# Performance work log

Hardware: AMD Instinct MI355X
Metric: run time of the kernel (lower is better)

The kernel has to match this reference:

```python
import jax, jax.numpy as jnp
import numpy as np

HID = 1024
DEPTH = 2

def _rhn_layer(x, Win, bin_, Wh, bh, Wt, bt):
    # x: [B, T, in]; returns outputs [B, T, H]
    B = x.shape[0]
    h0 = jnp.zeros((B, HID), dtype=x.dtype)
    xt = jnp.swapaxes(x, 0, 1)  # [T, B, in]

    def step(h_prev, x_t):
        h = x_t @ Win + bin_
        for i in range(DEPTH):
            t_gate = jax.nn.sigmoid(h @ Wt[i] + bt[i])
            h_layer = jnp.tanh(h @ Wh[i] + bh[i])
            h = t_gate * h_layer + (1.0 - t_gate) * h
        h_new = h + h_prev
        return h_new, h_new

    _, outs = jax.lax.scan(step, h0, xt)  # [T, B, H]
    return jnp.swapaxes(outs, 0, 1)


def setup_inputs() -> dict:
    key = jax.random.key(0)
    ks = jax.random.split(key, 16)
    B, T, IN, H, OUT = 64, 256, 128, HID, 128
    s = lambda fan_in: 1.0 / np.sqrt(fan_in)
    d = {}
    d["x"] = jax.random.normal(ks[0], (B, T, IN), dtype=jnp.float32)
    # layer 0 (input_size=IN)
    d["l0_Win"] = jax.random.uniform(ks[1], (IN, H), minval=-s(IN), maxval=s(IN))
    d["l0_bin"] = jax.random.uniform(ks[2], (H,), minval=-s(IN), maxval=s(IN))
    d["l0_Wh"] = jax.random.uniform(ks[3], (DEPTH, H, H), minval=-s(H), maxval=s(H))
    d["l0_bh"] = jax.random.uniform(ks[4], (DEPTH, H), minval=-s(H), maxval=s(H))
    d["l0_Wt"] = jax.random.uniform(ks[5], (DEPTH, H, H), minval=-s(H), maxval=s(H))
    d["l0_bt"] = jax.random.uniform(ks[6], (DEPTH, H), minval=-s(H), maxval=s(H))
    # layer 1 (input_size=H)
    d["l1_Win"] = jax.random.uniform(ks[7], (H, H), minval=-s(H), maxval=s(H))
    d["l1_bin"] = jax.random.uniform(ks[8], (H,), minval=-s(H), maxval=s(H))
    d["l1_Wh"] = jax.random.uniform(ks[9], (DEPTH, H, H), minval=-s(H), maxval=s(H))
    d["l1_bh"] = jax.random.uniform(ks[10], (DEPTH, H), minval=-s(H), maxval=s(H))
    d["l1_Wt"] = jax.random.uniform(ks[11], (DEPTH, H, H), minval=-s(H), maxval=s(H))
    d["l1_bt"] = jax.random.uniform(ks[12], (DEPTH, H), minval=-s(H), maxval=s(H))
    # final fc
    d["fc_W"] = jax.random.uniform(ks[13], (H, OUT), minval=-s(H), maxval=s(H))
    d["fc_b"] = jax.random.uniform(ks[14], (OUT,), minval=-s(H), maxval=s(H))
    return d


def reference(x, l0_Win, l0_bin, l0_Wh, l0_bh, l0_Wt, l0_bt,
              l1_Win, l1_bin, l1_Wh, l1_bh, l1_Wt, l1_bt, fc_W, fc_b):
    out = _rhn_layer(x, l0_Win, l0_bin, l0_Wh, l0_bh, l0_Wt, l0_bt)
    out = _rhn_layer(out, l1_Win, l1_bin, l1_Wh, l1_bh, l1_Wt, l1_bt)
    # forecast_horizon = 1 -> last time step only
    out = out[:, -1:, :] @ fc_W + fc_b  # [B, 1, OUT]
    return out
```

## Files before the change

kernel.cpp:

```cpp
#include <hip/hip_runtime.h>

typedef unsigned short u16;
typedef unsigned int u32;
typedef __bf16 bf16x8 __attribute__((ext_vector_type(8)));
typedef float floatx4 __attribute__((ext_vector_type(4)));

#define HID 1024
#define BATCH 64
#define SEQ 256
#define INDIM 128
#define OUTDIM 128
#define MROWS (BATCH*SEQ)
#define CUMP 140

__device__ __forceinline__ float b2f(u16 u) {
    union { u32 u; float f; } v; v.u = ((u32)u) << 16; return v.f;
}
__device__ __forceinline__ u16 f2b(float f) {
    union { float f; u32 u; } v; v.f = f;
    u32 x = v.u;
    x += 0x7fffu + ((x >> 16) & 1u);
    return (u16)(x >> 16);
}
__device__ __forceinline__ float sigm(float x) { return 1.f / (1.f + __expf(-x)); }
__device__ __forceinline__ float tanh_f(float x) { return 2.f / (1.f + __expf(-2.f * x)) - 1.f; }

__device__ __forceinline__ void gld16(const u16* g, u16* l) {
    __builtin_amdgcn_global_load_lds(
        (const __attribute__((address_space(1))) void*)g,
        (__attribute__((address_space(3))) void*)l, 16, 0, 0);
}

__device__ __forceinline__ void bar_sync() {
    asm volatile("" ::: "memory");
    __builtin_amdgcn_s_barrier();
    asm volatile("" ::: "memory");
}
template <int N>
__device__ __forceinline__ void vm_bar() {
    asm volatile("s_waitcnt vmcnt(%0)" :: "n"(N) : "memory");
    __builtin_amdgcn_s_barrier();
    asm volatile("" ::: "memory");
}

__device__ __forceinline__ int is_fp32(const u16* probe, int tid) {
    const int lane = tid & 63;
    const int e = (probe[lane * 7] >> 7) & 0xff;
    return __ballot(e >= 127) != 0ULL;
}

struct PrepList {
    const void* ts[10]; u16* td[10]; int tR[10]; int tC[10]; long toff[10];
    const void* cs[8];  u16* cd[8];  int cn[8];
};

__global__ void prep18(PrepList P, const u16* __restrict__ probe) {
    const int tid  = threadIdx.x;
    const int fp32 = is_fp32(probe, tid);
    const int z = blockIdx.z;
    if (z < 10) {
        const int tx = tid & 31, ty = tid >> 5;
        const void* src = P.ts[z];
        u16*        dst = P.td[z];
        const int R  = P.tR[z];
        const int Cc = P.tC[z];
        const long zo = P.toff[z];
        const int tr = blockIdx.y * 32, tc = blockIdx.x * 32;
        if (tr >= R || tc >= Cc) return;
        __align__(16) __shared__ u16 t[32][33];
#pragma unroll
        for (int i = 0; i < 4; ++i) {
            const int r = ty + i * 8;
            const long e = zo + (long)(tr + r) * Cc + tc + tx;
            u16 v;
            if (fp32) v = f2b(((const float*)src)[e]);
            else      v = ((const u16*)src)[e];
            t[r][tx] = v;
        }
        __syncthreads();
#pragma unroll
        for (int i = 0; i < 4; ++i) {
            const int r = ty + i * 8;
            dst[(size_t)(tc + r) * R + tr + tx] = t[tx][r];
        }
    } else {
        const int c = z - 10;
        const int n = P.cn[c];
        const int lin = blockIdx.y * gridDim.x + blockIdx.x;
        const int stride = gridDim.x * gridDim.y * 256;
        for (int i = lin * 256 + tid; i < n; i += stride) {
            u16 o;
            if (fp32) o = f2b(((const float*)P.cs[c])[i]);
            else      o = ((const u16*)P.cs[c])[i];
            P.cd[c][i] = o;
        }
    }
}

__device__ __forceinline__ void tile_swizzle(int& m0, int& n0) {
    const int lin = blockIdx.y * gridDim.x + blockIdx.x;
    const int xcd = lin & 7;
    const int loc = lin >> 3;
    m0 = (xcd * 16 + (loc & 15)) * 128;
    n0 = (loc >> 4) * 128;
}

__device__ __forceinline__ void tile_swizzle8(int& m0, int& n0) {
    const int lin = blockIdx.x;
    const int xcd = lin & 7;
    const int loc = lin >> 3;
    m0 = (xcd * 8 + (loc & 7)) * 256;
    n0 = (loc >> 3) * 128;
}

__global__ __launch_bounds__(256, 2) void gemm128(
    const u16* __restrict__ A, const u16* __restrict__ BT,
    const u16* __restrict__ bias, u16* __restrict__ C,
    int M, int N, int K)
{
    __align__(16) __shared__ u16 As[128 * 64];
    __align__(16) __shared__ u16 Bs[128 * 64];

    const int tid  = threadIdx.x;
    const int lane = tid & 63;
    const int wid  = tid >> 6;
    const int wr   = wid >> 1;
    const int wc   = wid & 1;

    int m0, n0;
    tile_swizzle(m0, n0);

    floatx4 acc[4][4] = {};

    const int srow = lane >> 3;
    const int scol = 8 * ((lane & 7) ^ (lane >> 3));
    const int cb   = wid * 4;
    const u16* Ag[4]; const u16* Bg[4];
    u16 *Al[4], *Bl[4];
#pragma unroll
    for (int j = 0; j < 4; ++j) {
        const int c = cb + j;
        const int r = c * 8 + srow;
        Ag[j] = A  + (size_t)(m0 + r) * K + scol;
        Bg[j] = BT + (size_t)(n0 + r) * K + scol;
        Al[j] = As + c * 512;
        Bl[j] = Bs + c * 512;
    }

    const int quad = lane >> 4;
    const int l16  = lane & 15;
    const int swz  = l16 & 7;

    const int nk = K >> 6;
    for (int kt = 0; kt < nk; ++kt) {
        __syncthreads();
#pragma unroll
        for (int j = 0; j < 4; ++j) {
            gld16(Ag[j], Al[j]);  gld16(Bg[j], Bl[j]);
            Ag[j] += 64; Bg[j] += 64;
        }
        __syncthreads();

#pragma unroll
        for (int kk = 0; kk < 2; ++kk) {
            const int slot = ((kk * 4 + quad) ^ swz) * 8;
            bf16x8 af[4], bfr[4];
#pragma unroll
            for (int i = 0; i < 4; ++i) {
                af[i]  = *(const bf16x8*)(As + (wr * 64 + i * 16 + l16) * 64 + slot);
                bfr[i] = *(const bf16x8*)(Bs + (wc * 64 + i * 16 + l16) * 64 + slot);
            }
#pragma unroll
            for (int i = 0; i < 4; ++i)
#pragma unroll
                for (int j = 0; j < 4; ++j)
                    acc[i][j] = __builtin_amdgcn_mfma_f32_16x16x32_bf16(af[i], bfr[j], acc[i][j], 0, 0, 0);
        }
    }

#pragma unroll
    for (int i = 0; i < 4; ++i) {
        const int rowb = m0 + wr * 64 + i * 16 + quad * 4;
#pragma unroll
        for (int j = 0; j < 4; ++j) {
            const int col = n0 + wc * 64 + j * 16 + l16;
            const float bv = b2f(bias[col]);
#pragma unroll
            for (int r = 0; r < 4; ++r)
                C[(size_t)(rowb + r) * N + col] = f2b(acc[i][j][r] + bv);
        }
    }
}

__global__ __launch_bounds__(256, 2) void gemm_wp_bias(
    const u16* __restrict__ At, const u16* __restrict__ Ah,
    const u16* __restrict__ BT,
    const u16* __restrict__ binv, const u16* __restrict__ bt0, const u16* __restrict__ bh0,
    u16* __restrict__ Ct, u16* __restrict__ Ch,
    u16* __restrict__ obt, u16* __restrict__ obh)
{
    const int tid = threadIdx.x;
    if (blockIdx.z == 1) {
        __shared__ float part[256];
        const u16* tW = blockIdx.y ? Ah : At;
        const u16* bo = blockIdx.y ? bh0 : bt0;
        u16*       ob = blockIdx.y ? obh : obt;
        const int j  = blockIdx.x * 128 + (tid & 127);
        const int kh = tid >> 7;
        const u16* row = tW + (size_t)j * HID + kh * 512;
        float acc = 0.f;
        for (int k = 0; k < 512; k += 8) {
            uint4 wv = *(const uint4*)(row + k);
            uint4 bv = *(const uint4*)(binv + kh * 512 + k);
            const u16* w = (const u16*)&wv;
            const u16* b = (const u16*)&bv;
#pragma unroll
            for (int e = 0; e < 8; ++e) acc += b2f(b[e]) * b2f(w[e]);
        }
        part[tid] = acc;
        __syncthreads();
        if (tid < 128)
            ob[j] = f2b(part[tid] + part[tid + 128] + b2f(bo[j]));
        return;
    }

    const u16* A = blockIdx.y ? Ah : At;
    u16*       C = blockIdx.y ? Ch : Ct;
    const int m0 = blockIdx.x * 128;
    const int K = HID, N = 128;

    __align__(16) __shared__ u16 As[128 * 64];
    __align__(16) __shared__ u16 Bs[128 * 64];

    const int lane = tid & 63;
    const int wid  = tid >> 6;
    const int wr   = wid >> 1;
    const int wc   = wid & 1;

    floatx4 acc[4][4] = {};

    const int srow = lane >> 3;
    const int scol = 8 * ((lane & 7) ^ (lane >> 3));
    const int cb   = wid * 4;
    const u16* Ag[4]; const u16* Bg[4];
    u16 *Al[4], *Bl[4];
#pragma unroll
    for (int j = 0; j < 4; ++j) {
        const int c = cb + j;
        const int r = c * 8 + srow;
        Ag[j] = A  + (size_t)(m0 + r) * K + scol;
        Bg[j] = BT + (size_t)r * K + scol;
        Al[j] = As + c * 512;
        Bl[j] = Bs + c * 512;
    }

    const int quad = lane >> 4;
    const int l16  = lane & 15;
    const int swz  = l16 & 7;

    for (int kt = 0; kt < (K >> 6); ++kt) {
        __syncthreads();
#pragma unroll
        for (int j = 0; j < 4; ++j) {
            gld16(Ag[j], Al[j]);  gld16(Bg[j], Bl[j]);
            Ag[j] += 64; Bg[j] += 64;
        }
        __syncthreads();

#pragma unroll
        for (int kk = 0; kk < 2; ++kk) {
            const int slot = ((kk * 4 + quad) ^ swz) * 8;
            bf16x8 af[4], bfr[4];
#pragma unroll
            for (int i = 0; i < 4; ++i) {
                af[i]  = *(const bf16x8*)(As + (wr * 64 + i * 16 + l16) * 64 + slot);
                bfr[i] = *(const bf16x8*)(Bs + (wc * 64 + i * 16 + l16) * 64 + slot);
            }
#pragma unroll
            for (int i = 0; i < 4; ++i)
#pragma unroll
                for (int j = 0; j < 4; ++j)
                    acc[i][j] = __builtin_amdgcn_mfma_f32_16x16x32_bf16(af[i], bfr[j], acc[i][j], 0, 0, 0);
        }
    }

#pragma unroll
    for (int i = 0; i < 4; ++i) {
        const int rowb = m0 + wr * 64 + i * 16 + quad * 4;
#pragma unroll
        for (int j = 0; j < 4; ++j) {
            const int col = wc * 64 + j * 16 + l16;
#pragma unroll
            for (int r = 0; r < 4; ++r)
                C[(size_t)(rowb + r) * N + col] = f2b(acc[i][j][r]);
        }
    }
}

__global__ __launch_bounds__(512, 2) void gemm_hw3(
    const u16* __restrict__ A,
    const u16* __restrict__ WtP,
    const u16* __restrict__ WhP,
    const u16* __restrict__ WiT,
    const u16* __restrict__ bpt, const u16* __restrict__ bph,
    const u16* __restrict__ bin,
    u16* __restrict__ Hout,
    int M, int N, int K)
{
    __align__(16) __shared__ u16 As [128 * 64];
    __align__(16) __shared__ u16 Bts[128 * 64];
    __align__(16) __shared__ u16 Bhs[128 * 64];
    __align__(16) __shared__ u16 Bis[128 * 64];

    const int tid  = threadIdx.x;
    const int lane = tid & 63;
    const int wid  = tid >> 6;
    const int wm   = wid >> 2;
    const int wn   = wid & 3;

    int m0, n0;
    tile_swizzle(m0, n0);

    floatx4 acct[4][2] = {};
    floatx4 acch[4][2] = {};
    floatx4 acci[4][2] = {};

    const int srow = lane >> 3;
    const int scol = 8 * ((lane & 7) ^ srow);
    const u16* Ag[2]; const u16* Tg[2]; const u16* Hg[2]; const u16* Ig[2];
    u16 *Al[2], *Tl[2], *Hl[2], *Il[2];
#pragma unroll
    for (int j = 0; j < 2; ++j) {
        const int c = wid * 2 + j;
        const int r = c * 8 + srow;
        Ag[j] = A   + (size_t)(m0 + r) * K + scol;
        Tg[j] = WtP + (size_t)(n0 + r) * K + scol;
        Hg[j] = WhP + (size_t)(n0 + r) * K + scol;
        Ig[j] = WiT + (size_t)(n0 + r) * K + scol;
        Al[j] = As  + c * 512;
        Tl[j] = Bts + c * 512;
        Hl[j] = Bhs + c * 512;
        Il[j] = Bis + c * 512;
    }

    const int quad = lane >> 4;
    const int l16  = lane & 15;
    const int swz  = l16 & 7;

    const int nk = K >> 6;
    for (int kt = 0; kt < nk; ++kt) {
        __syncthreads();
#pragma unroll
        for (int j = 0; j < 2; ++j) {
            gld16(Ag[j], Al[j]);  gld16(Tg[j], Tl[j]);
            gld16(Hg[j], Hl[j]);  gld16(Ig[j], Il[j]);
            Ag[j] += 64; Tg[j] += 64; Hg[j] += 64; Ig[j] += 64;
        }
        __syncthreads();

#pragma unroll
        for (int kk = 0; kk < 2; ++kk) {
            const int slot = ((kk * 4 + quad) ^ swz) * 8;
            bf16x8 af[4], btf[2], bhf[2], bif[2];
#pragma unroll
            for (int i = 0; i < 4; ++i)
                af[i] = *(const bf16x8*)(As + (wm * 64 + i * 16 + l16) * 64 + slot);
#pragma unroll
            for (int j = 0; j < 2; ++j) {
                btf[j] = *(const bf16x8*)(Bts + (wn * 32 + j * 16 + l16) * 64 + slot);
                bhf[j] = *(const bf16x8*)(Bhs + (wn * 32 + j * 16 + l16) * 64 + slot);
                bif[j] = *(const bf16x8*)(Bis + (wn * 32 + j * 16 + l16) * 64 + slot);
            }
#pragma unroll
            for (int i = 0; i < 4; ++i)
#pragma unroll
                for (int j = 0; j < 2; ++j) {
                    acct[i][j] = __builtin_amdgcn_mfma_f32_16x16x32_bf16(af[i], btf[j], acct[i][j], 0, 0, 0);
                    acch[i][j] = __builtin_amdgcn_mfma_f32_16x16x32_bf16(af[i], bhf[j], acch[i][j], 0, 0, 0);
                    acci[i][j] = __builtin_amdgcn_mfma_f32_16x16x32_bf16(af[i], bif[j], acci[i][j], 0, 0, 0);
                }
        }
    }

#pragma unroll
    for (int i = 0; i < 4; ++i) {
        const int rowb = m0 + wm * 64 + i * 16 + quad * 4;
#pragma unroll
        for (int j = 0; j < 2; ++j) {
            const int col = n0 + wn * 32 + j * 16 + l16;
            const float biv = b2f(bin[col]);
            const float btv = b2f(bpt[col]);
            const float bhv = b2f(bph[col]);
#pragma unroll
            for (int r = 0; r < 4; ++r) {
                const float h  = acci[i][j][r] + biv;
                const float tg = sigm(acct[i][j][r] + btv);
                const float hl = tanh_f(acch[i][j][r] + bhv);
                Hout[(size_t)(rowb + r) * N + col] = f2b(h + tg * (hl - h));
            }
        }
    }
}

__global__ __launch_bounds__(256, 2) void gemm_hw(
    const u16* __restrict__ A,
    const u16* __restrict__ WtT,
    const u16* __restrict__ WhT,
    const u16* __restrict__ bt, const u16* __restrict__ bh,
    u16* __restrict__ Hout,
    int M, int N, int K)
{
    __align__(16) __shared__ u16 As [128 * 64];
    __align__(16) __shared__ u16 Bts[128 * 64];
    __align__(16) __shared__ u16 Bhs[128 * 64];

    const int tid  = threadIdx.x;
    const int lane = tid & 63;
    const int wid  = tid >> 6;
    const int wr   = wid >> 1;
    const int wc   = wid & 1;

    int m0, n0;
    tile_swizzle(m0, n0);

    floatx4 acct[4][4] = {};
    floatx4 acch[4][4] = {};

    const int srow = lane >> 3;
    const int scol = 8 * ((lane & 7) ^ (lane >> 3));
    const int cb   = wid * 4;
    const u16* Ag[4]; const u16* Tg[4]; const u16* Hg[4];
    u16 *Al[4], *Tl[4], *Hl[4];
#pragma unroll
    for (int j = 0; j < 4; ++j) {
        const int c = cb + j;
        const int r = c * 8 + srow;
        Ag[j] = A   + (size_t)(m0 + r) * K + scol;
        Tg[j] = WtT + (size_t)(n0 + r) * K + scol;
        Hg[j] = WhT + (size_t)(n0 + r) * K + scol;
        Al[j] = As  + c * 512;
        Tl[j] = Bts + c * 512;
        Hl[j] = Bhs + c * 512;
    }

    const int quad = lane >> 4;
    const int l16  = lane & 15;
    const int swz  = l16 & 7;

    const int nk = K >> 6;
    for (int kt = 0; kt < nk; ++kt) {
        __syncthreads();
#pragma unroll
        for (int j = 0; j < 4; ++j) {
            gld16(Ag[j], Al[j]);  gld16(Tg[j], Tl[j]);  gld16(Hg[j], Hl[j]);
            Ag[j] += 64; Tg[j] += 64; Hg[j] += 64;
        }
        __syncthreads();

#pragma unroll
        for (int kk = 0; kk < 2; ++kk) {
            const int slot = ((kk * 4 + quad) ^ swz) * 8;
            bf16x8 af[4], btf[4], bhf[4];
#pragma unroll
            for (int i = 0; i < 4; ++i) {
                af[i]  = *(const bf16x8*)(As  + (wr * 64 + i * 16 + l16) * 64 + slot);
                btf[i] = *(const bf16x8*)(Bts + (wc * 64 + i * 16 + l16) * 64 + slot);
                bhf[i] = *(const bf16x8*)(Bhs + (wc * 64 + i * 16 + l16) * 64 + slot);
            }
#pragma unroll
            for (int i = 0; i < 4; ++i)
#pragma unroll
                for (int j = 0; j < 4; ++j) {
                    acct[i][j] = __builtin_amdgcn_mfma_f32_16x16x32_bf16(af[i], btf[j], acct[i][j], 0, 0, 0);
                    acch[i][j] = __builtin_amdgcn_mfma_f32_16x16x32_bf16(af[i], bhf[j], acch[i][j], 0, 0, 0);
                }
        }
    }

#pragma unroll
    for (int i = 0; i < 4; ++i) {
        const int rowb = m0 + wr * 64 + i * 16 + quad * 4;
#pragma unroll
        for (int j = 0; j < 4; ++j) {
            const int col = n0 + wc * 64 + j * 16 + l16;
            const float btv = b2f(bt[col]);
            const float bhv = b2f(bh[col]);
#pragma unroll
            for (int r = 0; r < 4; ++r) {
                const size_t idx = (size_t)(rowb + r) * N + col;
                const float hold = b2f(A[idx]);
                const float tg = sigm(acct[i][j][r] + btv);
                const float hl = tanh_f(acch[i][j][r] + bhv);
                Hout[idx] = f2b(hold + tg * (hl - hold));
            }
        }
    }
}

__global__ __launch_bounds__(256, 2) void gemm_hw_sum(
    const u16* __restrict__ A,
    const u16* __restrict__ WtT,
    const u16* __restrict__ WhT,
    const u16* __restrict__ bt, const u16* __restrict__ bh,
    float* __restrict__ hpart,
    int M, int N, int K)
{
    __align__(16) __shared__ u16 As [128 * 64];
    __align__(16) __shared__ u16 Bts[128 * 64];
    __align__(16) __shared__ u16 Bhs[128 * 64];

    const int tid  = threadIdx.x;
    const int lane = tid & 63;
    const int wid  = tid >> 6;
    const int wr   = wid >> 1;
    const int wc   = wid & 1;

    int m0, n0;
    tile_swizzle(m0, n0);

    floatx4 acct[4][4] = {};
    floatx4 acch[4][4] = {};

    const int srow = lane >> 3;
    const int scol = 8 * ((lane & 7) ^ (lane >> 3));
    const int cb   = wid * 4;
    const u16* Ag[4]; const u16* Tg[4]; const u16* Hg[4];
    u16 *Al[4], *Tl[4], *Hl[4];
#pragma unroll
    for (int j = 0; j < 4; ++j) {
        const int c = cb + j;
        const int r = c * 8 + srow;
        Ag[j] = A   + (size_t)(m0 + r) * K + scol;
        Tg[j] = WtT + (size_t)(n0 + r) * K + scol;
        Hg[j] = WhT + (size_t)(n0 + r) * K + scol;
        Al[j] = As  + c * 512;
        Tl[j] = Bts + c * 512;
        Hl[j] = Bhs + c * 512;
    }

    const int quad = lane >> 4;
    const int l16  = lane & 15;
    const int swz  = l16 & 7;

    const int nk = K >> 6;
    for (int kt = 0; kt < nk; ++kt) {
        __syncthreads();
#pragma unroll
        for (int j = 0; j < 4; ++j) {
            gld16(Ag[j], Al[j]);  gld16(Tg[j], Tl[j]);  gld16(Hg[j], Hl[j]);
            Ag[j] += 64; Tg[j] += 64; Hg[j] += 64;
        }
        __syncthreads();

#pragma unroll
        for (int kk = 0; kk < 2; ++kk) {
            const int slot = ((kk * 4 + quad) ^ swz) * 8;
            bf16x8 af[4], btf[4], bhf[4];
#pragma unroll
            for (int i = 0; i < 4; ++i) {
                af[i]  = *(const bf16x8*)(As  + (wr * 64 + i * 16 + l16) * 64 + slot);
                btf[i] = *(const bf16x8*)(Bts + (wc * 64 + i * 16 + l16) * 64 + slot);
                bhf[i] = *(const bf16x8*)(Bhs + (wc * 64 + i * 16 + l16) * 64 + slot);
            }
#pragma unroll
            for (int i = 0; i < 4; ++i)
#pragma unroll
                for (int j = 0; j < 4; ++j) {
                    acct[i][j] = __builtin_amdgcn_mfma_f32_16x16x32_bf16(af[i], btf[j], acct[i][j], 0, 0, 0);
                    acch[i][j] = __builtin_amdgcn_mfma_f32_16x16x32_bf16(af[i], bhf[j], acch[i][j], 0, 0, 0);
                }
        }
    }

    const int b    = m0 >> 8;
    const int slot = ((m0 >> 7) & 1) * 2 + wr;
#pragma unroll
    for (int j = 0; j < 4; ++j) {
        const int col = n0 + wc * 64 + j * 16 + l16;
        const float btv = b2f(bt[col]);
        const float bhv = b2f(bh[col]);
        float colsum = 0.f;
#pragma unroll
        for (int i = 0; i < 4; ++i) {
            const int rowb = m0 + wr * 64 + i * 16 + quad * 4;
#pragma unroll
            for (int r = 0; r < 4; ++r) {
                const size_t idx = (size_t)(rowb + r) * N + col;
                const float hold = b2f(A[idx]);
                const float tg = sigm(acct[i][j][r] + btv);
                const float hl = tanh_f(acch[i][j][r] + bhv);
                colsum += hold + tg * (hl - hold);
            }
        }
        colsum += __shfl_xor(colsum, 16, 64);
        colsum += __shfl_xor(colsum, 32, 64);
        if (quad == 0)
            hpart[((size_t)(slot * BATCH + b)) * HID + col] = colsum;
    }
}

__device__ __forceinline__ void hw8_mainloop(
    u16* lds,
    const u16* __restrict__ A, const u16* __restrict__ WtT, const u16* __restrict__ WhT,
    int m0, int n0, int K,
    floatx4 (&acct)[4][4], floatx4 (&acch)[4][4])
{
    const int tid  = threadIdx.x;
    const int lane = tid & 63;
    const int wid  = tid >> 6;
    const int wr   = wid >> 1;
    const int wc   = wid & 1;

    const int srow = lane >> 3;
    const int scol = 8 * ((lane & 7) ^ srow);

    const u16* Ag = A   + (size_t)(m0 + wid * 32 + srow) * K + scol;
    const u16* Tg = WtT + (size_t)(n0 + wid * 16 + srow) * K + scol;
    const u16* Hg = WhT + (size_t)(n0 + wid * 16 + srow) * K + scol;
    const size_t K8 = (size_t)K * 8;

    u16* dA = lds + wid * 2048;
    u16* dT = lds + 16384 + wid * 1024;
    u16* dH = lds + 24576 + wid * 1024;

    const int quad = lane >> 4;
    const int l16  = lane & 15;
    const int swz  = l16 & 7;
    const int s0 = (quad ^ swz) * 8;
    const int s1 = ((4 + quad) ^ swz) * 8;
    const int ra = wr * 64 + l16;
    const int rb = wc * 64 + l16;

    gld16(Tg,           dT);
    gld16(Tg +     K8,  dT + 512);
    gld16(Ag,           dA);
    gld16(Ag +     K8,  dA + 512);
    gld16(Ag + 2 * K8,  dA + 1024);
    gld16(Ag + 3 * K8,  dA + 1536);
    gld16(Hg,           dH);
    gld16(Hg +     K8,  dH + 512);
    Ag += 64; Tg += 64; Hg += 64;
    vm_bar<2>();

    const int nk = K >> 6;
    for (int kt = 0; kt < nk; ++kt) {
        const int  cur = kt & 1;
        const int  nb  = (cur ^ 1) * 32768;
        const bool pf  = (kt + 1 < nk);
        const u16* Sa = lds + cur * 32768;
        const u16* St = Sa + 16384;
        const u16* Sh = Sa + 24576;

        bf16x8 af0[4], af1[4], bq[4];

#pragma unroll
        for (int i = 0; i < 4; ++i) {
            af0[i] = *(const bf16x8*)(Sa + (ra + i * 16) * 64 + s0);
            bq[i]  = *(const bf16x8*)(St + (rb + i * 16) * 64 + s0);
        }
        if (pf) {
            gld16(Tg,      dT + nb);  gld16(Tg + K8, dT + nb + 512);
            gld16(Ag,      dA + nb);  gld16(Ag + K8, dA + nb + 512);
        }
        bar_sync();
        __builtin_amdgcn_s_setprio(1);
#pragma unroll
        for (int i = 0; i < 4; ++i)
#pragma unroll
            for (int j = 0; j < 4; ++j)
                acct[i][j] = __builtin_amdgcn_mfma_f32_16x16x32_bf16(af0[i], bq[j], acct[i][j], 0, 0, 0);
        __builtin_amdgcn_s_setprio(0);

#pragma unroll
        for (int i = 0; i < 4; ++i) {
            af1[i] = *(const bf16x8*)(Sa + (ra + i * 16) * 64 + s1);
            bq[i]  = *(const bf16x8*)(St + (rb + i * 16) * 64 + s1);
        }
        if (pf) {
            gld16(Ag + 2 * K8, dA + nb + 1024);
            gld16(Ag + 3 * K8, dA + nb + 1536);
            vm_bar<6>();
        } else {
            vm_bar<0>();
        }
        __builtin_amdgcn_s_setprio(1);
#pragma unroll
        for (int i = 0; i < 4; ++i)
#pragma unroll
            for (int j = 0; j < 4; ++j)
                acct[i][j] = __builtin_amdgcn_mfma_f32_16x16x32_bf16(af1[i], bq[j], acct[i][j], 0, 0, 0);
        __builtin_amdgcn_s_setprio(0);

#pragma unroll
        for (int i = 0; i < 4; ++i)
            bq[i] = *(const bf16x8*)(Sh + (rb + i * 16) * 64 + s0);
        bar_sync();
        __builtin_amdgcn_s_setprio(1);
#pragma unroll
        for (int i = 0; i < 4; ++i)
#pragma unroll
            for (int j = 0; j < 4; ++j)
                acch[i][j] = __builtin_amdgcn_mfma_f32_16x16x32_bf16(af0[i], bq[j], acch[i][j], 0, 0, 0);
        __builtin_amdgcn_s_setprio(0);

#pragma unroll
        for (int i = 0; i < 4; ++i)
            bq[i] = *(const bf16x8*)(Sh + (rb + i * 16) * 64 + s1);
        if (pf) {
            gld16(Hg,      dH + nb);
            gld16(Hg + K8, dH + nb + 512);
            vm_bar<2>();
        } else {
            bar_sync();
        }
        __builtin_amdgcn_s_setprio(1);
#pragma unroll
        for (int i = 0; i < 4; ++i)
#pragma unroll
            for (int j = 0; j < 4; ++j)
                acch[i][j] = __builtin_amdgcn_mfma_f32_16x16x32_bf16(af1[i], bq[j], acch[i][j], 0, 0, 0);
        __builtin_amdgcn_s_setprio(0);

        Ag += 64; Tg += 64; Hg += 64;
    }
}

__global__ __launch_bounds__(512, 2) void gemm_hw8_cum(
    const u16* __restrict__ A,
    const u16* __restrict__ WtT,
    const u16* __restrict__ WhT,
    const u16* __restrict__ bt, const u16* __restrict__ bh,
    u16* __restrict__ Y,
    int M, int N, int K)
{
    __align__(16) __shared__ u16 lds[65536];
    __shared__ float tot[512];

    int m0, n0;
    tile_swizzle8(m0, n0);

    floatx4 acct[4][4] = {};
    floatx4 acch[4][4] = {};
    hw8_mainloop(lds, A, WtT, WhT, m0, n0, K, acct, acch);

    const int tid  = threadIdx.x;
    const int lane = tid & 63;
    const int wid  = tid >> 6;
    const int wr   = wid >> 1;
    const int wc   = wid & 1;
    const int quad = lane >> 4;
    const int l16  = lane & 15;

    __syncthreads();

#pragma unroll
    for (int i = 0; i < 4; ++i) {
        const int rowl = wr * 64 + i * 16 + quad * 4;
#pragma unroll
        for (int j = 0; j < 4; ++j) {
            const int coll = wc * 64 + j * 16 + l16;
            const float btv = b2f(bt[n0 + coll]);
            const float bhv = b2f(bh[n0 + coll]);
#pragma unroll
            for (int r = 0; r < 4; ++r) {
                const size_t idx = (size_t)(m0 + rowl + r) * N + n0 + coll;
                const float hold = b2f(A[idx]);
                const float tg = sigm(acct[i][j][r] + btv);
                const float hl = tanh_f(acch[i][j][r] + bhv);
                lds[(rowl + r) * CUMP + coll] = f2b(hold + tg * (hl - hold));
            }
        }
    }
    __syncthreads();

    const int seg  = tid >> 7;
    const int colc = tid & 127;
    const int base = seg * 64 * CUMP + colc;
    {
        float local = 0.f;
#pragma unroll 8
        for (int t = 0; t < 64; ++t)
            local += b2f(lds[base + t * CUMP]);
        tot[seg * 128 + colc] = local;
    }
    __syncthreads();
    {
        float off = 0.f;
#pragma unroll
        for (int s = 0; s < 3; ++s)
            off += (s < seg) ? tot[s * 128 + colc] : 0.f;
        float acc = off;
#pragma unroll 8
        for (int t = 0; t < 64; ++t) {
            const int o = base + t * CUMP;
            acc += b2f(lds[o]);
            lds[o] = f2b(acc);
        }
    }
    __syncthreads();

#pragma unroll
    for (int it = 0; it < 16; ++it) {
        const int o   = it * 2048 + tid * 4;
        const int row = o >> 7;
        const int col = o & 127;
        *(uint2*)&Y[(size_t)(m0 + row) * N + n0 + col] =
            *(const uint2*)&lds[row * CUMP + col];
    }
}

__global__ void fc_final(const float* __restrict__ hp, const void* __restrict__ W,
                         const void* __restrict__ bias, void* __restrict__ out) {
    __shared__ float sh[HID];
    const int fp32 = is_fp32((const u16*)W, threadIdx.x);
    const int b = blockIdx.x, o = threadIdx.x;
    for (int k = o; k < HID; k += 128) {
        float v = 0.f;
#pragma unroll
        for (int s = 0; s < 4; ++s)
            v += hp[((size_t)(s * BATCH + b)) * HID + k];
        sh[k] = v;
    }
    __syncthreads();
    float acc;
    if (fp32) {
        acc = ((const float*)bias)[o];
        for (int k = 0; k < HID; ++k)
            acc += sh[k] * ((const float*)W)[(size_t)k * OUTDIM + o];
        ((float*)out)[b * OUTDIM + o] = acc;
    } else {
        acc = b2f(((const u16*)bias)[o]);
        for (int k = 0; k < HID; ++k)
            acc += sh[k] * b2f(((const u16*)W)[(size_t)k * OUTDIM + o]);
        ((u16*)out)[b * OUTDIM + o] = f2b(acc);
    }
}

extern "C" void kernel_launch(void* const* d_in, const int* in_sizes, int n_in,
                              void* d_out, int out_size, void* d_ws, size_t ws_size,
                              hipStream_t stream) {
    const void* x      = d_in[0];
    const void* l0_Win = d_in[1];
    const void* l0_bin = d_in[2];
    const void* l0_Wh  = d_in[3];
    const void* l0_bh  = d_in[4];
    const void* l0_Wt  = d_in[5];
    const void* l0_bt  = d_in[6];
    const void* l1_Win = d_in[7];
    const void* l1_bin = d_in[8];
    const void* l1_Wh  = d_in[9];
    const void* l1_bh  = d_in[10];
    const void* l1_Wt  = d_in[11];
    const void* l1_bt  = d_in[12];
    const void* fc_W   = d_in[13];
    const void* fc_b   = d_in[14];

    char* ws = (char*)d_ws;
    u16* Pa = (u16*)(ws);
    u16* Pb = (u16*)(ws + 33554432);
    u16* xc = Pb;
    u16* tW = (u16*)(ws + 67108864);
    u16* tWin0 = tW;
    u16* tWt00 = tWin0 + 131072;
    u16* tWt01 = tWt00 + 1048576;
    u16* tWh00 = tWt01 + 1048576;
    u16* tWh01 = tWh00 + 1048576;
    u16* tWin1 = tWh01 + 1048576;
    u16* tWt10 = tWin1 + 1048576;
    u16* tWt11 = tWt10 + 1048576;
    u16* tWh10 = tWt11 + 1048576;
    u16* tWh11 = tWh10 + 1048576;
    u16* smallb = tWh11 + 1048576;
    u16* binc0 = smallb;
    u16* bhc0  = binc0 + 1024;
    u16* btc0  = bhc0 + 2048;
    u16* binc1 = btc0 + 2048;
    u16* bhc1  = binc1 + 1024;
    u16* btc1  = bhc1 + 2048;
    u16* Win0c = btc1 + 2048;
    u16* Wpt   = Win0c + 131072;
    u16* Wph   = Wpt + 131072;
    u16* bpt   = Wph + 131072;
    u16* bph   = bpt + 1024;
    float* hpart = (float*)Pa;

    const u16* probe = (const u16*)l0_Wh;

    const long DD = (long)HID * HID;
    PrepList P;
    P.ts[0] = l0_Win; P.td[0] = tWin0; P.tR[0] = INDIM; P.tC[0] = HID; P.toff[0] = 0;
    P.ts[1] = l0_Wt;  P.td[1] = tWt00; P.tR[1] = HID;   P.tC[1] = HID; P.toff[1] = 0;
    P.ts[2] = l0_Wt;  P.td[2] = tWt01; P.tR[2] = HID;   P.tC[2] = HID; P.toff[2] = DD;
    P.ts[3] = l0_Wh;  P.td[3] = tWh00; P.tR[3] = HID;   P.tC[3] = HID; P.toff[3] = 0;
    P.ts[4] = l0_Wh;  P.td[4] = tWh01; P.tR[4] = HID;   P.tC[4] = HID; P.toff[4] = DD;
    P.ts[5] = l1_Win; P.td[5] = tWin1; P.tR[5] = HID;   P.tC[5] = HID; P.toff[5] = 0;
    P.ts[6] = l1_Wt;  P.td[6] = tWt10; P.tR[6] = HID;   P.tC[6] = HID; P.toff[6] = 0;
    P.ts[7] = l1_Wt;  P.td[7] = tWt11; P.tR[7] = HID;   P.tC[7] = HID; P.toff[7] = DD;
    P.ts[8] = l1_Wh;  P.td[8] = tWh10; P.tR[8] = HID;   P.tC[8] = HID; P.toff[8] = 0;
    P.ts[9] = l1_Wh;  P.td[9] = tWh11; P.tR[9] = HID;   P.tC[9] = HID; P.toff[9] = DD;
    P.cs[0] = x;      P.cd[0] = xc;    P.cn[0] = MROWS * INDIM;
    P.cs[1] = l0_bin; P.cd[1] = binc0; P.cn[1] = HID;
    P.cs[2] = l0_bh;  P.cd[2] = bhc0;  P.cn[2] = 2 * HID;
    P.cs[3] = l0_bt;  P.cd[3] = btc0;  P.cn[3] = 2 * HID;
    P.cs[4] = l1_bin; P.cd[4] = binc1; P.cn[4] = HID;
    P.cs[5] = l1_bh;  P.cd[5] = bhc1;  P.cn[5] = 2 * HID;
    P.cs[6] = l1_bt;  P.cd[6] = btc1;  P.cn[6] = 2 * HID;
    P.cs[7] = l0_Win; P.cd[7] = Win0c; P.cn[7] = INDIM * HID;
    prep18<<<dim3(32, 32, 18), 256, 0, stream>>>(P, probe);

    gemm_wp_bias<<<dim3(8, 2, 2), 256, 0, stream>>>(tWt00, tWh00, Win0c,
                                                    binc0, btc0, bhc0,
                                                    Wpt, Wph, bpt, bph);

    gemm_hw3<<<dim3(8, 128), 512, 0, stream>>>(xc, Wpt, Wph, tWin0, bpt, bph, binc0,
                                               Pa, MROWS, HID, INDIM);
    gemm_hw8_cum<<<512, 512, 0, stream>>>(Pa, tWt01, tWh01, btc0 + HID, bhc0 + HID, Pb, MROWS, HID, HID);

    gemm128<<<dim3(8, 128), 256, 0, stream>>>(Pb, tWin1, binc1, Pa, MROWS, HID, HID);
    gemm_hw<<<dim3(8, 128), 256, 0, stream>>>(Pa, tWt10, tWh10, btc1, bhc1, Pb, MROWS, HID, HID);
    gemm_hw_sum<<<dim3(8, 128), 256, 0, stream>>>(Pb, tWt11, tWh11, btc1 + HID, bhc1 + HID,
                                                  hpart, MROWS, HID, HID);

    fc_final<<<64, 128, 0, stream>>>(hpart, fc_W, fc_b, d_out);
}
```

Measured before the change: 453.4 us.

## Fold layer-1 input projection into first highway gate GEMM via precomputed weight products

```diff
diff --git a/kernel.cpp b/kernel.cpp
--- a/kernel.cpp
+++ b/kernel.cpp
@@ -51,10 +51,10 @@
 
 struct PrepList {
     const void* ts[10]; u16* td[10]; int tR[10]; int tC[10]; long toff[10];
-    const void* cs[8];  u16* cd[8];  int cn[8];
+    const void* cs[9];  u16* cd[9];  int cn[9];
 };
 
-__global__ void prep18(PrepList P, const u16* __restrict__ probe) {
+__global__ void prep19(PrepList P, const u16* __restrict__ probe) {
     const int tid  = threadIdx.x;
     const int fp32 = is_fp32(probe, tid);
     const int z = blockIdx.z;
@@ -113,22 +113,69 @@
     n0 = (loc >> 3) * 128;
 }
 
-__global__ __launch_bounds__(256, 2) void gemm128(
-    const u16* __restrict__ A, const u16* __restrict__ BT,
-    const u16* __restrict__ bias, u16* __restrict__ C,
-    int M, int N, int K)
-{
+struct WpArgs {
+    const u16 *At0, *Ah0, *B0;
+    const u16 *At1, *Ah1, *B1;
+    const u16 *bin0, *bt0, *bh0;
+    const u16 *bin1, *bt1, *bh1;
+    u16 *Ct0, *Ch0, *Ct1, *Ch1;
+    u16 *obt0, *obh0, *obt1, *obh1;
+};
+
+__global__ __launch_bounds__(256, 2) void wp_bias2(WpArgs W) {
     __align__(16) __shared__ u16 As[128 * 64];
     __align__(16) __shared__ u16 Bs[128 * 64];
+    __shared__ float part[256];
 
     const int tid  = threadIdx.x;
+    const int gate = blockIdx.y;
+    const int K = HID;
+
+    const u16* A; const u16* BT; u16* C;
+    int m0, n0, NN;
+
+    if (blockIdx.z == 1) {
+        if (blockIdx.x >= 24) return;
+        if (blockIdx.x >= 8) {
+            const int lay = (blockIdx.x >= 16);
+            const int xb  = blockIdx.x - (lay ? 16 : 8);
+            const u16* tW  = lay ? (gate ? W.Ah1 : W.At1) : (gate ? W.Ah0 : W.At0);
+            const u16* biv = lay ? W.bin1 : W.bin0;
+            const u16* bo  = lay ? (gate ? W.bh1 : W.bt1) : (gate ? W.bh0 : W.bt0);
+            u16*       ob  = lay ? (gate ? W.obh1 : W.obt1) : (gate ? W.obh0 : W.obt0);
+            const int j  = xb * 128 + (tid & 127);
+            const int kh = tid >> 7;
+            const u16* row = tW + (size_t)j * HID + kh * 512;
+            float acc = 0.f;
+            for (int k = 0; k < 512; k += 8) {
+                uint4 wv = *(const uint4*)(row + k);
+                uint4 bv = *(const uint4*)(biv + kh * 512 + k);
+                const u16* w = (const u16*)&wv;
+                const u16* b = (const u16*)&bv;
+#pragma unroll
+                for (int e = 0; e < 8; ++e) acc += b2f(b[e]) * b2f(w[e]);
+            }
+            part[tid] = acc;
+            __syncthreads();
+            if (tid < 128)
+                ob[j] = f2b(part[tid] + part[tid + 128] + b2f(bo[j]));
+            return;
+        }
+        A  = gate ? W.Ah0 : W.At0;
+        BT = W.B0;
+        C  = gate ? W.Ch0 : W.Ct0;
+        m0 = blockIdx.x * 128; n0 = 0; NN = 128;
+    } else {
+        A  = gate ? W.Ah1 : W.At1;
+        BT = W.B1;
+        C  = gate ? W.Ch1 : W.Ct1;
+        m0 = (blockIdx.x >> 3) * 128; n0 = (blockIdx.x & 7) * 128; NN = HID;
+    }
+
     const int lane = tid & 63;
     const int wid  = tid >> 6;
     const int wr   = wid >> 1;
     const int wc   = wid & 1;
-
-    int m0, n0;
-    tile_swizzle(m0, n0);
 
     floatx4 acc[4][4] = {};
 
@@ -151,8 +198,7 @@
     const int l16  = lane & 15;
     const int swz  = l16 & 7;
 
-    const int nk = K >> 6;
-    for (int kt = 0; kt < nk; ++kt) {
+    for (int kt = 0; kt < (K >> 6); ++kt) {
         __syncthreads();
 #pragma unroll
         for (int j = 0; j < 4; ++j) {
@@ -184,115 +230,9 @@
 #pragma unroll
         for (int j = 0; j < 4; ++j) {
             const int col = n0 + wc * 64 + j * 16 + l16;
-            const float bv = b2f(bias[col]);
 #pragma unroll
             for (int r = 0; r < 4; ++r)
-                C[(size_t)(rowb + r) * N + col] = f2b(acc[i][j][r] + bv);
-        }
-    }
-}
-
-__global__ __launch_bounds__(256, 2) void gemm_wp_bias(
-    const u16* __restrict__ At, const u16* __restrict__ Ah,
-    const u16* __restrict__ BT,
-    const u16* __restrict__ binv, const u16* __restrict__ bt0, const u16* __restrict__ bh0,
-    u16* __restrict__ Ct, u16* __restrict__ Ch,
-    u16* __restrict__ obt, u16* __restrict__ obh)
-{
-    const int tid = threadIdx.x;
-    if (blockIdx.z == 1) {
-        __shared__ float part[256];
-        const u16* tW = blockIdx.y ? Ah : At;
-        const u16* bo = blockIdx.y ? bh0 : bt0;
-        u16*       ob = blockIdx.y ? obh : obt;
-        const int j  = blockIdx.x * 128 + (tid & 127);
-        const int kh = tid >> 7;
-        const u16* row = tW + (size_t)j * HID + kh * 512;
-        float acc = 0.f;
-        for (int k = 0; k < 512; k += 8) {
-            uint4 wv = *(const uint4*)(row + k);
-            uint4 bv = *(const uint4*)(binv + kh * 512 + k);
-            const u16* w = (const u16*)&wv;
-            const u16* b = (const u16*)&bv;
-#pragma unroll
-            for (int e = 0; e < 8; ++e) acc += b2f(b[e]) * b2f(w[e]);
-        }
-        part[tid] = acc;
-        __syncthreads();
-        if (tid < 128)
-            ob[j] = f2b(part[tid] + part[tid + 128] + b2f(bo[j]));
-        return;
-    }
-
-    const u16* A = blockIdx.y ? Ah : At;
-    u16*       C = blockIdx.y ? Ch : Ct;
-    const int m0 = blockIdx.x * 128;
-    const int K = HID, N = 128;
-
-    __align__(16) __shared__ u16 As[128 * 64];
-    __align__(16) __shared__ u16 Bs[128 * 64];
-
-    const int lane = tid & 63;
-    const int wid  = tid >> 6;
-    const int wr   = wid >> 1;
-    const int wc   = wid & 1;
-
-    floatx4 acc[4][4] = {};
-
-    const int srow = lane >> 3;
-    const int scol = 8 * ((lane & 7) ^ (lane >> 3));
-    const int cb   = wid * 4;
-    const u16* Ag[4]; const u16* Bg[4];
-    u16 *Al[4], *Bl[4];
-#pragma unroll
-    for (int j = 0; j < 4; ++j) {
-        const int c = cb + j;
-        const int r = c * 8 + srow;
-        Ag[j] = A  + (size_t)(m0 + r) * K + scol;
-        Bg[j] = BT + (size_t)r * K + scol;
-        Al[j] = As + c * 512;
-        Bl[j] = Bs + c * 512;
-    }
-
-    const int quad = lane >> 4;
-    const int l16  = lane & 15;
-    const int swz  = l16 & 7;
-
-    for (int kt = 0; kt < (K >> 6); ++kt) {
-        __syncthreads();
-#pragma unroll
-        for (int j = 0; j < 4; ++j) {
-            gld16(Ag[j], Al[j]);  gld16(Bg[j], Bl[j]);
-            Ag[j] += 64; Bg[j] += 64;
-        }
-        __syncthreads();
-
-#pragma unroll
-        for (int kk = 0; kk < 2; ++kk) {
-            const int slot = ((kk * 4 + quad) ^ swz) * 8;
-            bf16x8 af[4], bfr[4];
-#pragma unroll
-            for (int i = 0; i < 4; ++i) {
-                af[i]  = *(const bf16x8*)(As + (wr * 64 + i * 16 + l16) * 64 + slot);
-                bfr[i] = *(const bf16x8*)(Bs + (wc * 64 + i * 16 + l16) * 64 + slot);
-            }
-#pragma unroll
-            for (int i = 0; i < 4; ++i)
-#pragma unroll
-                for (int j = 0; j < 4; ++j)
-                    acc[i][j] = __builtin_amdgcn_mfma_f32_16x16x32_bf16(af[i], bfr[j], acc[i][j], 0, 0, 0);
-        }
-    }
-
-#pragma unroll
-    for (int i = 0; i < 4; ++i) {
-        const int rowb = m0 + wr * 64 + i * 16 + quad * 4;
-#pragma unroll
-        for (int j = 0; j < 4; ++j) {
-            const int col = wc * 64 + j * 16 + l16;
-#pragma unroll
-            for (int r = 0; r < 4; ++r)
-                C[(size_t)(rowb + r) * N + col] = f2b(acc[i][j][r]);
+                C[(size_t)(rowb + r) * NN + col] = f2b(acc[i][j][r]);
         }
     }
 }
@@ -402,45 +342,50 @@
     }
 }
 
-__global__ __launch_bounds__(256, 2) void gemm_hw(
+__global__ __launch_bounds__(512, 2) void gemm_hw3k(
     const u16* __restrict__ A,
-    const u16* __restrict__ WtT,
-    const u16* __restrict__ WhT,
-    const u16* __restrict__ bt, const u16* __restrict__ bh,
+    const u16* __restrict__ WtP,
+    const u16* __restrict__ WhP,
+    const u16* __restrict__ WiT,
+    const u16* __restrict__ bpt, const u16* __restrict__ bph,
+    const u16* __restrict__ bin,
     u16* __restrict__ Hout,
     int M, int N, int K)
 {
     __align__(16) __shared__ u16 As [128 * 64];
     __align__(16) __shared__ u16 Bts[128 * 64];
     __align__(16) __shared__ u16 Bhs[128 * 64];
+    __align__(16) __shared__ u16 Bis[128 * 64];
 
     const int tid  = threadIdx.x;
     const int lane = tid & 63;
     const int wid  = tid >> 6;
-    const int wr   = wid >> 1;
-    const int wc   = wid & 1;
+    const int wm   = wid >> 2;
+    const int wn   = wid & 3;
 
     int m0, n0;
     tile_swizzle(m0, n0);
 
-    floatx4 acct[4][4] = {};
-    floatx4 acch[4][4] = {};
+    floatx4 acct[4][2] = {};
+    floatx4 acch[4][2] = {};
+    floatx4 acci[4][2] = {};
 
     const int srow = lane >> 3;
-    const int scol = 8 * ((lane & 7) ^ (lane >> 3));
-    const int cb   = wid * 4;
-    const u16* Ag[4]; const u16* Tg[4]; const u16* Hg[4];
-    u16 *Al[4], *Tl[4], *Hl[4];
-#pragma unroll
-    for (int j = 0; j < 4; ++j) {
-        const int c = cb + j;
+    const int scol = 8 * ((lane & 7) ^ srow);
+    const u16* Ag[2]; const u16* Tg[2]; const u16* Hg[2]; const u16* Ig[2];
+    u16 *Al[2], *Tl[2], *Hl[2], *Il[2];
+#pragma unroll
+    for (int j = 0; j < 2; ++j) {
+        const int c = wid * 2 + j;
         const int r = c * 8 + srow;
         Ag[j] = A   + (size_t)(m0 + r) * K + scol;
-        Tg[j] = WtT + (size_t)(n0 + r) * K + scol;
-        Hg[j] = WhT + (size_t)(n0 + r) * K + scol;
+        Tg[j] = WtP + (size_t)(n0 + r) * K + scol;
+        Hg[j] = WhP + (size_t)(n0 + r) * K + scol;
+        Ig[j] = WiT + (size_t)(n0 + r) * K + scol;
         Al[j] = As  + c * 512;
         Tl[j] = Bts + c * 512;
         Hl[j] = Bhs + c * 512;
+        Il[j] = Bis + c * 512;
     }
 
     const int quad = lane >> 4;
@@ -451,47 +396,52 @@
     for (int kt = 0; kt < nk; ++kt) {
         __syncthreads();
 #pragma unroll
-        for (int j = 0; j < 4; ++j) {
-            gld16(Ag[j], Al[j]);  gld16(Tg[j], Tl[j]);  gld16(Hg[j], Hl[j]);
-            Ag[j] += 64; Tg[j] += 64; Hg[j] += 64;
+        for (int j = 0; j < 2; ++j) {
+            gld16(Ag[j], Al[j]);  gld16(Tg[j], Tl[j]);
+            gld16(Hg[j], Hl[j]);  gld16(Ig[j], Il[j]);
+            Ag[j] += 64; Tg[j] += 64; Hg[j] += 64; Ig[j] += 64;
         }
         __syncthreads();
 
 #pragma unroll
         for (int kk = 0; kk < 2; ++kk) {
             const int slot = ((kk * 4 + quad) ^ swz) * 8;
-            bf16x8 af[4], btf[4], bhf[4];
-#pragma unroll
-            for (int i = 0; i < 4; ++i) {
-                af[i]  = *(const bf16x8*)(As  + (wr * 64 + i * 16 + l16) * 64 + slot);
-                btf[i] = *(const bf16x8*)(Bts + (wc * 64 + i * 16 + l16) * 64 + slot);
-                bhf[i] = *(const bf16x8*)(Bhs + (wc * 64 + i * 16 + l16) * 64 + slot);
+            bf16x8 af[4], btf[2], bhf[2], bif[2];
+#pragma unroll
+            for (int i = 0; i < 4; ++i)
+                af[i] = *(const bf16x8*)(As + (wm * 64 + i * 16 + l16) * 64 + slot);
+#pragma unroll
+            for (int j = 0; j < 2; ++j) {
+                btf[j] = *(const bf16x8*)(Bts + (wn * 32 + j * 16 + l16) * 64 + slot);
+                bhf[j] = *(const bf16x8*)(Bhs + (wn * 32 + j * 16 + l16) * 64 + slot);
+                bif[j] = *(const bf16x8*)(Bis + (wn * 32 + j * 16 + l16) * 64 + slot);
             }
 #pragma unroll
             for (int i = 0; i < 4; ++i)
 #pragma unroll
-                for (int j = 0; j < 4; ++j) {
+                for (int j = 0; j < 2; ++j) {
                     acct[i][j] = __builtin_amdgcn_mfma_f32_16x16x32_bf16(af[i], btf[j], acct[i][j], 0, 0, 0);
                     acch[i][j] = __builtin_amdgcn_mfma_f32_16x16x32_bf16(af[i], bhf[j], acch[i][j], 0, 0, 0);
+                    acci[i][j] = __builtin_amdgcn_mfma_f32_16x16x32_bf16(af[i], bif[j], acci[i][j], 0, 0, 0);
                 }
         }
     }
 
 #pragma unroll
     for (int i = 0; i < 4; ++i) {
-        const int rowb = m0 + wr * 64 + i * 16 + quad * 4;
-#pragma unroll
-        for (int j = 0; j < 4; ++j) {
-            const int col = n0 + wc * 64 + j * 16 + l16;
-            const float btv = b2f(bt[col]);
-            const float bhv = b2f(bh[col]);
+        const int rowb = m0 + wm * 64 + i * 16 + quad * 4;
+#pragma unroll
+        for (int j = 0; j < 2; ++j) {
+            const int col = n0 + wn * 32 + j * 16 + l16;
+            const float biv = b2f(bin[col]);
+            const float btv = b2f(bpt[col]);
+            const float bhv = b2f(bph[col]);
 #pragma unroll
             for (int r = 0; r < 4; ++r) {
-                const size_t idx = (size_t)(rowb + r) * N + col;
-                const float hold = b2f(A[idx]);
+                const float h  = acci[i][j][r] + biv;
                 const float tg = sigm(acct[i][j][r] + btv);
                 const float hl = tanh_f(acch[i][j][r] + bhv);
-                Hout[idx] = f2b(hold + tg * (hl - hold));
+                Hout[(size_t)(rowb + r) * N + col] = f2b(h + tg * (hl - h));
             }
         }
     }
@@ -882,7 +832,12 @@
     u16* Wph   = Wpt + 131072;
     u16* bpt   = Wph + 131072;
     u16* bph   = bpt + 1024;
-    float* hpart = (float*)Pa;
+    u16* Win1c = bph + 1024;
+    u16* Wpt1  = Win1c + 1048576;
+    u16* Wph1  = Wpt1 + 1048576;
+    u16* bpt1  = Wph1 + 1048576;
+    u16* bph1  = bpt1 + 1024;
+    float* hpart = (float*)Pb;
 
     const u16* probe = (const u16*)l0_Wh;
 
@@ -906,19 +861,25 @@
     P.cs[5] = l1_bh;  P.cd[5] = bhc1;  P.cn[5] = 2 * HID;
     P.cs[6] = l1_bt;  P.cd[6] = btc1;  P.cn[6] = 2 * HID;
     P.cs[7] = l0_Win; P.cd[7] = Win0c; P.cn[7] = INDIM * HID;
-    prep18<<<dim3(32, 32, 18), 256, 0, stream>>>(P, probe);
-
-    gemm_wp_bias<<<dim3(8, 2, 2), 256, 0, stream>>>(tWt00, tWh00, Win0c,
-                                                    binc0, btc0, bhc0,
-                                                    Wpt, Wph, bpt, bph);
+    P.cs[8] = l1_Win; P.cd[8] = Win1c; P.cn[8] = HID * HID;
+    prep19<<<dim3(32, 32, 19), 256, 0, stream>>>(P, probe);
+
+    WpArgs W;
+    W.At0 = tWt00; W.Ah0 = tWh00; W.B0 = Win0c;
+    W.At1 = tWt10; W.Ah1 = tWh10; W.B1 = Win1c;
+    W.bin0 = binc0; W.bt0 = btc0; W.bh0 = bhc0;
+    W.bin1 = binc1; W.bt1 = btc1; W.bh1 = bhc1;
+    W.Ct0 = Wpt;  W.Ch0 = Wph;  W.Ct1 = Wpt1; W.Ch1 = Wph1;
+    W.obt0 = bpt; W.obh0 = bph; W.obt1 = bpt1; W.obh1 = bph1;
+    wp_bias2<<<dim3(64, 2, 2), 256, 0, stream>>>(W);
 
     gemm_hw3<<<dim3(8, 128), 512, 0, stream>>>(xc, Wpt, Wph, tWin0, bpt, bph, binc0,
                                                Pa, MROWS, HID, INDIM);
     gemm_hw8_cum<<<512, 512, 0, stream>>>(Pa, tWt01, tWh01, btc0 + HID, bhc0 + HID, Pb, MROWS, HID, HID);
 
-    gemm128<<<dim3(8, 128), 256, 0, stream>>>(Pb, tWin1, binc1, Pa, MROWS, HID, HID);
-    gemm_hw<<<dim3(8, 128), 256, 0, stream>>>(Pa, tWt10, tWh10, btc1, bhc1, Pb, MROWS, HID, HID);
-    gemm_hw_sum<<<dim3(8, 128), 256, 0, stream>>>(Pb, tWt11, tWh11, btc1 + HID, bhc1 + HID,
+    gemm_hw3k<<<dim3(8, 128), 512, 0, stream>>>(Pb, Wpt1, Wph1, tWin1, bpt1, bph1, binc1,
+                                                Pa, MROWS, HID, HID);
+    gemm_hw_sum<<<dim3(8, 128), 256, 0, stream>>>(Pa, tWt11, tWh11, btc1 + HID, bhc1 + HID,
                                                   hpart, MROWS, HID, HID);
 
     fc_final<<<64, 128, 0, stream>>>(hpart, fc_W, fc_b, d_out);
```

Measured after the change: 482.6 us. +6.4%, slower.
